# Kernel tuning notes

Hardware: AMD Instinct MI355X
Metric: run time of the kernel (lower is better)

## Reference

```python
import jax, jax.numpy as jnp
import numpy as np

B, N, D, H, L = 16, 1024, 256, 128, 2  # batch, nodes, feat dim, gcn_hidden, n_layers (D == 2*H)


def setup_inputs() -> dict:
    key = jax.random.key(0)
    ks = jax.random.split(key, 16)
    inp = {
        "gcn_input": jax.random.normal(ks[0], (B, N, D), jnp.float32),
        # scale adjacencies by 1/N so aggregated features stay O(1)
        "latent_adj": jax.random.uniform(ks[1], (B, N, N), jnp.float32) / N,
        "dep_adj": jax.random.uniform(ks[2], (B, N, N), jnp.float32) / N,
        # stacked per-layer parameters (leading dim L); layers share shapes since D == 2*H
        "refine_gate": jax.random.normal(ks[3], (L, D, 1), jnp.float32) * 0.02,
        "gate_W_in": jax.random.normal(ks[4], (L, D, 1), jnp.float32) * 0.02,
        "gate_b_in": jnp.zeros((L, 1), jnp.float32),
        "gate_W_out": jax.random.normal(ks[5], (L, D, 1), jnp.float32) * 0.02,
        "gate_b_out": jnp.zeros((L, 1), jnp.float32),
        "fc_in_W": jax.random.normal(ks[6], (L, H, D), jnp.float32) * 0.02,
        "fc_in_b": jnp.zeros((L, H), jnp.float32),
        "fc_out_W": jax.random.normal(ks[7], (L, H, D), jnp.float32) * 0.02,
        "fc_out_b": jnp.zeros((L, H), jnp.float32),
        "ln_g": jnp.ones((L, 2 * H), jnp.float32),
        "ln_b": jnp.zeros((L, 2 * H), jnp.float32),
    }
    return inp


def _gcn_layer(x, latent, dep, rg, Wgi, bgi, Wgo, bgo, Wi, bi, Wo, bo, g, b):
    # refine gate blends dependency and latent adjacency per source node
    gate = jax.nn.sigmoid(x @ rg)  # [B,N,1]
    A_in = gate * dep + (1.0 - gate) * latent  # [B,N,N]
    A_out = gate * jnp.swapaxes(dep, -1, -2) + (1.0 - gate) * jnp.swapaxes(latent, -1, -2)
    Ax_in = A_in @ x   # [B,N,D]
    Ax_out = A_out @ x
    # gcn gates (scalar bias added after the gated product, as in torch)
    Ax_in = Ax_in * jax.nn.sigmoid(Ax_in @ Wgi) + bgi
    Ax_out = Ax_out * jax.nn.sigmoid(Ax_out @ Wgo) + bgo
    # rec_fc(Ax) + rec_fc(x): weight applied to sum, bias counted twice (faithful)
    h_in = (Ax_in + x) @ Wi.T + 2.0 * bi   # [B,N,H]
    h_out = (Ax_out + x) @ Wo.T + 2.0 * bo
    h = jnp.concatenate([h_in, h_out], axis=-1)  # [B,N,2H]
    mu = jnp.mean(h, axis=-1, keepdims=True)
    var = jnp.var(h, axis=-1, keepdims=True)
    h = (h - mu) * jax.lax.rsqrt(var + 1e-5) * g + b
    return jax.nn.gelu(h, approximate=False)


def reference(gcn_input, latent_adj, dep_adj, refine_gate, gate_W_in, gate_b_in,
              gate_W_out, gate_b_out, fc_in_W, fc_in_b, fc_out_W, fc_out_b, ln_g, ln_b):
    x = gcn_input
    for l in range(refine_gate.shape[0]):  # small fixed layer count
        x = _gcn_layer(x, latent_adj, dep_adj, refine_gate[l],
                       gate_W_in[l], gate_b_in[l], gate_W_out[l], gate_b_out[l],
                       fc_in_W[l], fc_in_b[l], fc_out_W[l], fc_out_b[l],
                       ln_g[l], ln_b[l])
    return x
```

## Files before the change

### kernel.cpp

```cpp
#include <hip/hip_runtime.h>
#include <hip/hip_bf16.h>
#include <cstdint>

#define B_ 16
#define N_ 1024
#define D_ 256
#define H_ 128

typedef unsigned short u16;
typedef __attribute__((ext_vector_type(8))) short bf16x8;
typedef __attribute__((ext_vector_type(4))) short bf16x4;
typedef __attribute__((ext_vector_type(4))) float f32x4;

template<int V> struct IC { static constexpr int value = V; };

__device__ __forceinline__ u16 f2bf(float f) {
    union { float f; uint32_t u; } v; v.f = f;
    return (u16)((v.u + 0x7FFFu + ((v.u >> 16) & 1u)) >> 16);
}
__device__ __forceinline__ float bf2f(u16 h) {
    union { uint32_t u; float f; } v; v.u = ((uint32_t)h) << 16;
    return v.f;
}

typedef __attribute__((address_space(3))) void lds_void;
typedef const __attribute__((address_space(1))) void g_void;

__device__ __forceinline__ void gl_lds16(const void* g, void* l) {
    __builtin_amdgcn_global_load_lds((g_void*)g, (lds_void*)l, 16, 0, 0);
}

__device__ __forceinline__ void vm_wait6() { asm volatile("s_waitcnt vmcnt(6)" ::: "memory"); }
__device__ __forceinline__ void vm_wait3() { asm volatile("s_waitcnt vmcnt(3)" ::: "memory"); }
__device__ __forceinline__ void vm_wait2() { asm volatile("s_waitcnt vmcnt(2)" ::: "memory"); }
__device__ __forceinline__ void vm_wait0() { asm volatile("s_waitcnt vmcnt(0)" ::: "memory"); }
__device__ __forceinline__ void lgkm0()   { asm volatile("s_waitcnt lgkmcnt(0)" ::: "memory"); }
__device__ __forceinline__ void schedb()  { __builtin_amdgcn_sched_barrier(0); }

__global__ __launch_bounds__(256) void k_conv_adj(
    const float* __restrict__ dep, const float* __restrict__ lat,
    u16* __restrict__ depTb, u16* __restrict__ latTb)
{
    __shared__ u16 tile[64][64];
    const int bz = blockIdx.z;
    const int b = bz >> 1;
    const float* src = (bz & 1) ? lat : dep;
    u16* dstT = (bz & 1) ? latTb : depTb;
    const int r0 = blockIdx.y * 64, c0 = blockIdx.x * 64;
    const int t = threadIdx.x;
    const int r = t >> 2, cg = (t & 3) * 16;

    const float* srow = src + ((size_t)b * N_ + r0 + r) * N_ + c0 + cg;
    bf16x8 lo, hi;
    {
        const float4 v0 = *(const float4*)(srow);
        const float4 v1 = *(const float4*)(srow + 4);
        const float4 v2 = *(const float4*)(srow + 8);
        const float4 v3 = *(const float4*)(srow + 12);
        lo[0] = (short)f2bf(v0.x); lo[1] = (short)f2bf(v0.y); lo[2] = (short)f2bf(v0.z); lo[3] = (short)f2bf(v0.w);
        lo[4] = (short)f2bf(v1.x); lo[5] = (short)f2bf(v1.y); lo[6] = (short)f2bf(v1.z); lo[7] = (short)f2bf(v1.w);
        hi[0] = (short)f2bf(v2.x); hi[1] = (short)f2bf(v2.y); hi[2] = (short)f2bf(v2.z); hi[3] = (short)f2bf(v2.w);
        hi[4] = (short)f2bf(v3.x); hi[5] = (short)f2bf(v3.y); hi[6] = (short)f2bf(v3.z); hi[7] = (short)f2bf(v3.w);
    }

    const int g0 = (t & 3) * 2;
    const int s = r & 7;
    *(bf16x8*)(&tile[r][((g0    ) ^ s) * 8]) = lo;
    *(bf16x8*)(&tile[r][((g0 + 1) ^ s) * 8]) = hi;
    __syncthreads();

    const int sc = t >> 2, rg2 = (t & 3) * 16;
    bf16x8 o0, o1;
    #pragma unroll
    for (int i = 0; i < 8; ++i) {
        const int R = rg2 + i;
        o0[i] = (short)tile[R][(((sc >> 3) ^ (R & 7)) * 8) + (sc & 7)];
    }
    #pragma unroll
    for (int i = 0; i < 8; ++i) {
        const int R = rg2 + 8 + i;
        o1[i] = (short)tile[R][(((sc >> 3) ^ (R & 7)) * 8) + (sc & 7)];
    }
    u16* dT = dstT + ((size_t)b * N_ + c0 + sc) * N_ + r0 + rg2;
    *(bf16x8*)dT = o0;
    *(bf16x8*)(dT + 8) = o1;
}

__global__ __launch_bounds__(256) void k_gate_xt(
    const float* __restrict__ x, const float* __restrict__ rg,
    float* __restrict__ gate, u16* __restrict__ xT,
    const float* __restrict__ wi, const float* __restrict__ wo,
    u16* __restrict__ wib, u16* __restrict__ wob)
{
    if (blockIdx.y >= B_) {
        const int i = ((blockIdx.y - B_) * 32 + blockIdx.x) * 256 + threadIdx.x;
        wib[i] = f2bf(wi[i]);
        wob[i] = f2bf(wo[i]);
        return;
    }

    __shared__ u16 lx[D_][36];
    __shared__ float srg[D_];
    const int b = blockIdx.y, n0 = blockIdx.x * 32;
    const int t = threadIdx.x;
    srg[t] = rg[t];
    __syncthreads();

    const int r = t >> 3, cg = t & 7;
    const float* xrow = x + ((size_t)b * N_ + n0 + r) * D_;
    float dot = 0.f;
    #pragma unroll
    for (int u = 0; u < 8; ++u) {
        const int c = cg * 32 + u * 4;
        const float4 v = *(const float4*)(xrow + c);
        lx[c][r] = f2bf(v.x); lx[c + 1][r] = f2bf(v.y);
        lx[c + 2][r] = f2bf(v.z); lx[c + 3][r] = f2bf(v.w);
        dot += v.x * srg[c] + v.y * srg[c + 1] + v.z * srg[c + 2] + v.w * srg[c + 3];
    }
    dot += __shfl_down(dot, 4, 8);
    dot += __shfl_down(dot, 2, 8);
    dot += __shfl_down(dot, 1, 8);
    if (cg == 0) gate[(size_t)b * N_ + n0 + r] = 1.f / (1.f + expf(-dot));
    __syncthreads();

    #pragma unroll
    for (int i = 0; i < 8; ++i) {
        const int unit = i * 256 + t;
        const int d = unit >> 3, nch = (unit & 7) * 4;
        ushort4 wv;
        wv.x = lx[d][nch];     wv.y = lx[d][nch + 1];
        wv.z = lx[d][nch + 2]; wv.w = lx[d][nch + 3];
        *(ushort4*)(xT + ((size_t)b * D_ + d) * N_ + n0 + nch) = wv;
    }
}

__global__ __launch_bounds__(512, 2) void k_gemm_ax(
    const float* __restrict__ depf, const float* __restrict__ latf,
    const u16* __restrict__ depTb, const u16* __restrict__ latTb,
    const u16* __restrict__ xT,
    const float* __restrict__ gate,
    const float* __restrict__ Wgi, const float* __restrict__ Wgo,
    const float* __restrict__ bgi, const float* __restrict__ bgo,
    const float* __restrict__ xcur,
    u16* __restrict__ axin, u16* __restrict__ axout)
{
    __shared__ __align__(16) char smem[51712];
    u16* const sb = (u16*)smem;
    float* hbuf = (float*)smem;
    float* psum = (float*)(smem + 49152);
    float* sh_s = (float*)(smem + 51200);

    const int bid = blockIdx.x;
    const int logical = (bid & 7) * 32 + (bid >> 3);
    const int b = logical >> 4;
    const int rem = logical & 15;
    const int z = rem >> 3;
    const int m0 = (rem & 7) * 128;

    const float* Wg = z ? Wgo : Wgi;
    const float bg0 = z ? bgo[0] : bgi[0];
    u16* outp = z ? axout : axin;

    const int t = threadIdx.x;
    const int lane = t & 63;
    const int w = t >> 6;
    const int wr = w >> 2, wc = w & 3;

    const int arow = t >> 2;
    const int akq = t & 3;
    const float gv = gate[(size_t)b * N_ + m0 + arow];
    const int awoff = arow * 32 + ((akq ^ ((arow >> 1) & 3)) << 3);
    const float* gD = depf + ((size_t)b * N_ + m0 + arow) * N_ + akq * 8;
    const float* gL = latf + ((size_t)b * N_ + m0 + arow) * N_ + akq * 8;
    const u16* gT1 = depTb + ((size_t)b * N_ + m0 + arow) * N_ + akq * 8;
    const u16* gT2 = latTb + ((size_t)b * N_ + m0 + arow) * N_ + akq * 8;

    const int rl = lane >> 2;
    const int kk = (((lane & 3) ^ ((lane >> 3) & 3)) << 3);
    const u16* gB0 = xT + ((size_t)b * D_ + (w * 2) * 16 + rl) * N_ + kk;
    const u16* gB1 = xT + ((size_t)b * D_ + (w * 2 + 1) * 16 + rl) * N_ + kk;
    const int boff0 = 4096 + (w * 2) * 512;
    const int boff1 = 4096 + (w * 2 + 1) * 512;

    const int mrow = lane & 15;
    const int hi = lane >> 4;
    const int kg = (((lane >> 4) ^ ((mrow >> 1) & 3)) << 3);

    f32x4 acc[4][4];
    const f32x4 fz = {0.f, 0.f, 0.f, 0.f};
    #pragma unroll
    for (int i = 0; i < 4; ++i)
        #pragma unroll
        for (int j = 0; j < 4; ++j) acc[i][j] = fz;

    struct RegsF { float4 d0, d1, l0, l1; };
    struct RegsH { bf16x4 a0, a1, b0, b1; };

    auto run = [&](auto zc) {
        constexpr int Z = decltype(zc)::value;

        auto LOAD = [&](auto& r, int ks) {
            if constexpr (Z == 0) {
                r.d0 = *(const float4*)(gD + ks * 32);
                r.d1 = *(const float4*)(gD + ks * 32 + 4);
                r.l0 = *(const float4*)(gL + ks * 32);
                r.l1 = *(const float4*)(gL + ks * 32 + 4);
            } else {
                r.a0 = *(const bf16x4*)(gT1 + ks * 32);
                r.a1 = *(const bf16x4*)(gT1 + ks * 32 + 4);
                r.b0 = *(const bf16x4*)(gT2 + ks * 32);
                r.b1 = *(const bf16x4*)(gT2 + ks * 32 + 4);
            }
        };
        auto BLEND = [&](const auto& r, u16* dst) {
            bf16x8 bl;
            if constexpr (Z == 0) {
                bl[0] = (short)f2bf(r.l0.x + gv * (r.d0.x - r.l0.x));
                bl[1] = (short)f2bf(r.l0.y + gv * (r.d0.y - r.l0.y));
                bl[2] = (short)f2bf(r.l0.z + gv * (r.d0.z - r.l0.z));
                bl[3] = (short)f2bf(r.l0.w + gv * (r.d0.w - r.l0.w));
                bl[4] = (short)f2bf(r.l1.x + gv * (r.d1.x - r.l1.x));
                bl[5] = (short)f2bf(r.l1.y + gv * (r.d1.y - r.l1.y));
                bl[6] = (short)f2bf(r.l1.z + gv * (r.d1.z - r.l1.z));
                bl[7] = (short)f2bf(r.l1.w + gv * (r.d1.w - r.l1.w));
            } else {
                #pragma unroll
                for (int u = 0; u < 4; ++u) {
                    const float f1 = bf2f((u16)r.a0[u]);
                    const float f2 = bf2f((u16)r.b0[u]);
                    bl[u] = (short)f2bf(f2 + gv * (f1 - f2));
                }
                #pragma unroll
                for (int u = 0; u < 4; ++u) {
                    const float f1 = bf2f((u16)r.a1[u]);
                    const float f2 = bf2f((u16)r.b1[u]);
                    bl[4 + u] = (short)f2bf(f2 + gv * (f1 - f2));
                }
            }
            *(bf16x8*)dst = bl;
        };

        auto body = [&](int ks, auto& c, auto& n) {
            if (ks <= 28) LOAD(n, ks + 3);
            const u16* sA = sb + (ks & 1) * 12288;
            const u16* sBc = sA + 4096;
            bf16x8 a[4], fbv[4];
            #pragma unroll
            for (int mt = 0; mt < 4; ++mt)
                a[mt] = *(const bf16x8*)(sA + (wr * 64 + mt * 16 + mrow) * 32 + kg);
            #pragma unroll
            for (int nt = 0; nt < 4; ++nt)
                fbv[nt] = *(const bf16x8*)(sBc + (wc * 64 + nt * 16 + mrow) * 32 + kg);
            #pragma unroll
            for (int mt = 0; mt < 4; ++mt)
                #pragma unroll
                for (int nt = 0; nt < 4; ++nt)
                    acc[mt][nt] = __builtin_amdgcn_mfma_f32_16x16x32_bf16(a[mt], fbv[nt], acc[mt][nt], 0, 0, 0);
            schedb();
            __builtin_amdgcn_s_barrier();
            schedb();
            if (ks <= 29) {
                u16* cb = sb + (ks & 1) * 12288;
                BLEND(c, cb + awoff);
                gl_lds16(gB0 + (ks + 2) * 32, cb + boff0);
                gl_lds16(gB1 + (ks + 2) * 32, cb + boff1);
            }
            if (ks <= 28) vm_wait6();
            else if (ks == 29) vm_wait2();
            else if (ks == 30) vm_wait0();
            lgkm0();
            schedb();
            __builtin_amdgcn_s_barrier();
            schedb();
        };

        typename std::conditional<Z == 0, RegsF, RegsH>::type x, y;
        LOAD(x, 0); BLEND(x, sb + awoff);
        LOAD(y, 1); BLEND(y, sb + 12288 + awoff);
        LOAD(x, 2);
        gl_lds16(gB0, sb + boff0);          gl_lds16(gB1, sb + boff1);
        gl_lds16(gB0 + 32, sb + 12288 + boff0); gl_lds16(gB1 + 32, sb + 12288 + boff1);
        vm_wait2();
        lgkm0();
        schedb(); __builtin_amdgcn_s_barrier(); schedb();

        for (int kp = 0; kp < 16; ++kp) {
            body(2 * kp, x, y);
            body(2 * kp + 1, y, x);
        }
    };
    if (z == 0) run(IC<0>()); else run(IC<1>());
    __syncthreads();

    float wgv[4];
    #pragma unroll
    for (int nt = 0; nt < 4; ++nt) wgv[nt] = Wg[wc * 64 + nt * 16 + mrow];
    #pragma unroll
    for (int mt = 0; mt < 4; ++mt) {
        #pragma unroll
        for (int rr = 0; rr < 4; ++rr) {
            float p = acc[mt][0][rr] * wgv[0] + acc[mt][1][rr] * wgv[1]
                    + acc[mt][2][rr] * wgv[2] + acc[mt][3][rr] * wgv[3];
            p += __shfl_xor(p, 1, 16);
            p += __shfl_xor(p, 2, 16);
            p += __shfl_xor(p, 4, 16);
            p += __shfl_xor(p, 8, 16);
            if (mrow == 0) psum[(wr * 64 + mt * 16 + hi * 4 + rr) * 4 + wc] = p;
        }
    }
    __syncthreads();
    if (t < 128) {
        const float d = psum[t * 4] + psum[t * 4 + 1] + psum[t * 4 + 2] + psum[t * 4 + 3];
        sh_s[t] = 1.f / (1.f + expf(-d));
    }
    __syncthreads();

    #pragma unroll
    for (int p = 0; p < 4; ++p) {
        if (wr == (p >> 1)) {
            #pragma unroll
            for (int mtl = 0; mtl < 2; ++mtl) {
                const int mt = (p & 1) * 2 + mtl;
                #pragma unroll
                for (int nt = 0; nt < 4; ++nt) {
                    const int col = wc * 64 + nt * 16 + mrow;
                    #pragma unroll
                    for (int rr = 0; rr < 4; ++rr) {
                        const int hrow = mtl * 16 + hi * 4 + rr;
                        hbuf[hrow * 260 + col] = acc[mt][nt][rr];
                    }
                }
            }
        }
        __syncthreads();
        {
            const int sr = t >> 4;
            const int sc0 = (t & 15) * 16;
            const int grow = p * 32 + sr;
            const float s = sh_s[grow];
            const size_t gb = ((size_t)b * N_ + m0 + grow) * D_ + sc0;
            const float* xr = xcur + gb;
            u16* orow = outp + gb;
            bf16x8 o0, o1;
            #pragma unroll
            for (int u = 0; u < 8; ++u)
                o0[u] = (short)f2bf(hbuf[sr * 260 + sc0 + u] * s + bg0 + xr[u]);
            #pragma unroll
            for (int u = 0; u < 8; ++u)
                o1[u] = (short)f2bf(hbuf[sr * 260 + sc0 + 8 + u] * s + bg0 + xr[8 + u]);
            *(bf16x8*)orow = o0;
            *(bf16x8*)(orow + 8) = o1;
        }
        __syncthreads();
    }
}

__global__ __launch_bounds__(512, 2) void k_fc_ln(
    const u16* __restrict__ axin, const u16* __restrict__ axout,
    const u16* __restrict__ Wib, const u16* __restrict__ Wob,
    const float* __restrict__ bi, const float* __restrict__ bo,
    const float* __restrict__ lg, const float* __restrict__ lb,
    float* __restrict__ outp)
{
    __shared__ __align__(16) char smem[51712];
    u16* const sb = (u16*)smem;
    float* hbuf = (float*)smem;
    float* psum = (float*)(smem + 49152);
    float* sh_mu = (float*)(smem + 51200);
    float* sh_rs = (float*)(smem + 51456);

    const int bid = blockIdx.x;
    const int logical = (bid & 7) * 32 + (bid >> 3);
    const int b = logical >> 4;
    const int m0 = (logical & 15) * 64;

    const int t = threadIdx.x, lane = t & 63, w = t >> 6;
    const int wr = w >> 2, wc = w & 3;
    const int half = wc >> 1;

    const int rl = lane >> 2;
    const int kk = (((lane & 3) ^ ((lane >> 3) & 3)) << 3);

    const u16* gsrc[3];
    int loff[3];
    #pragma unroll
    for (int ci = 0; ci < 3; ++ci) {
        const int c = w * 3 + ci;
        if (c < 4) {
            gsrc[ci] = axin + ((size_t)b * N_ + m0 + c * 16 + rl) * D_ + kk;
            loff[ci] = c * 512;
        } else if (c < 8) {
            gsrc[ci] = axout + ((size_t)b * N_ + m0 + (c - 4) * 16 + rl) * D_ + kk;
            loff[ci] = 2048 + (c - 4) * 512;
        } else {
            const int cw = c - 8;
            const u16* base = (cw < 8) ? (Wib + (size_t)(cw * 16 + rl) * D_)
                                       : (Wob + (size_t)((cw - 8) * 16 + rl) * D_);
            gsrc[ci] = base + kk;
            loff[ci] = 4096 + cw * 512;
        }
    }

    f32x4 acc[2][4];
    const f32x4 fz = {0.f, 0.f, 0.f, 0.f};
    #pragma unroll
    for (int i = 0; i < 2; ++i)
        #pragma unroll
        for (int j = 0; j < 4; ++j) acc[i][j] = fz;

    #pragma unroll
    for (int ci = 0; ci < 3; ++ci) gl_lds16(gsrc[ci], sb + loff[ci]);
    #pragma unroll
    for (int ci = 0; ci < 3; ++ci) gl_lds16(gsrc[ci] + 32, sb + 12288 + loff[ci]);
    vm_wait3();
    lgkm0();
    schedb(); __builtin_amdgcn_s_barrier(); schedb();

    const int mrow = lane & 15;
    const int hi = lane >> 4;
    const int kg = (((lane >> 4) ^ ((mrow >> 1) & 3)) << 3);

    for (int ks = 0; ks < 8; ++ks) {
        const u16* cur = sb + (ks & 1) * 12288;
        const u16* sA = cur + (half ? 2048 : 0);
        const u16* sW = cur + 4096;
        bf16x8 a[2], fbv[4];
        #pragma unroll
        for (int mt = 0; mt < 2; ++mt)
            a[mt] = *(const bf16x8*)(sA + (wr * 32 + mt * 16 + mrow) * 32 + kg);
        #pragma unroll
        for (int nt = 0; nt < 4; ++nt)
            fbv[nt] = *(const bf16x8*)(sW + (wc * 64 + nt * 16 + mrow) * 32 + kg);
        #pragma unroll
        for (int mt = 0; mt < 2; ++mt)
            #pragma unroll
            for (int nt = 0; nt < 4; ++nt)
                acc[mt][nt] = __builtin_amdgcn_mfma_f32_16x16x32_bf16(a[mt], fbv[nt], acc[mt][nt], 0, 0, 0);
        schedb();
        __builtin_amdgcn_s_barrier();
        schedb();
        if (ks <= 5) {
            u16* nb = sb + (ks & 1) * 12288;
            #pragma unroll
            for (int ci = 0; ci < 3; ++ci) gl_lds16(gsrc[ci] + (ks + 2) * 32, nb + loff[ci]);
        }
        if (ks <= 5) vm_wait3();
        else if (ks == 6) vm_wait0();
        lgkm0();
        schedb();
        __builtin_amdgcn_s_barrier();
        schedb();
    }
    __syncthreads();

    float bc[4];
    #pragma unroll
    for (int nt = 0; nt < 4; ++nt) {
        const int colh = wc * 64 + nt * 16 + mrow;
        bc[nt] = 2.f * (colh < 128 ? bi[colh] : bo[colh - 128]);
    }
    #pragma unroll
    for (int mt = 0; mt < 2; ++mt)
        #pragma unroll
        for (int rr = 0; rr < 4; ++rr) {
            const int lrow = wr * 32 + mt * 16 + hi * 4 + rr;
            float s = 0.f, ss = 0.f;
            #pragma unroll
            for (int nt = 0; nt < 4; ++nt) {
                const float v = acc[mt][nt][rr] + bc[nt];
                s += v; ss += v * v;
            }
            s += __shfl_xor(s, 1, 16);  ss += __shfl_xor(ss, 1, 16);
            s += __shfl_xor(s, 2, 16);  ss += __shfl_xor(ss, 2, 16);
            s += __shfl_xor(s, 4, 16);  ss += __shfl_xor(ss, 4, 16);
            s += __shfl_xor(s, 8, 16);  ss += __shfl_xor(ss, 8, 16);
            if (mrow == 0) {
                psum[lrow * 8 + wc * 2] = s;
                psum[lrow * 8 + wc * 2 + 1] = ss;
            }
        }
    __syncthreads();
    if (t < 64) {
        const float s = psum[t * 8] + psum[t * 8 + 2] + psum[t * 8 + 4] + psum[t * 8 + 6];
        const float ss = psum[t * 8 + 1] + psum[t * 8 + 3] + psum[t * 8 + 5] + psum[t * 8 + 7];
        const float mu = s * (1.f / 256.f);
        const float var = ss * (1.f / 256.f) - mu * mu;
        sh_mu[t] = mu;
        sh_rs[t] = rsqrtf(var + 1e-5f);
    }
    __syncthreads();

    #pragma unroll
    for (int p = 0; p < 2; ++p) {
        if (wr == p) {
            #pragma unroll
            for (int mt = 0; mt < 2; ++mt)
                #pragma unroll
                for (int nt = 0; nt < 4; ++nt) {
                    const int col = wc * 64 + nt * 16 + mrow;
                    #pragma unroll
                    for (int rr = 0; rr < 4; ++rr) {
                        const int hrow = mt * 16 + hi * 4 + rr;
                        hbuf[hrow * 260 + col] = acc[mt][nt][rr] + bc[nt];
                    }
                }
        }
        __syncthreads();
        {
            const int sr = t >> 4;
            const int sc0 = (t & 15) * 16;
            const int grow = p * 32 + sr;
            const float mu = sh_mu[grow], rs = sh_rs[grow];
            float* orow = outp + ((size_t)b * N_ + m0 + grow) * D_ + sc0;
            #pragma unroll
            for (int q = 0; q < 4; ++q) {
                const float4 gg = *(const float4*)(lg + sc0 + q * 4);
                const float4 bb = *(const float4*)(lb + sc0 + q * 4);
                float4 o;
                const float v0 = (hbuf[sr * 260 + sc0 + q * 4    ] - mu) * rs * gg.x + bb.x;
                const float v1 = (hbuf[sr * 260 + sc0 + q * 4 + 1] - mu) * rs * gg.y + bb.y;
                const float v2 = (hbuf[sr * 260 + sc0 + q * 4 + 2] - mu) * rs * gg.z + bb.z;
                const float v3 = (hbuf[sr * 260 + sc0 + q * 4 + 3] - mu) * rs * gg.w + bb.w;
                o.x = 0.5f * v0 * (1.f + erff(v0 * 0.70710678118654752f));
                o.y = 0.5f * v1 * (1.f + erff(v1 * 0.70710678118654752f));
                o.z = 0.5f * v2 * (1.f + erff(v2 * 0.70710678118654752f));
                o.w = 0.5f * v3 * (1.f + erff(v3 * 0.70710678118654752f));
                *(float4*)(orow + q * 4) = o;
            }
        }
        __syncthreads();
    }
}

extern "C" void kernel_launch(void* const* d_in, const int* in_sizes, int n_in,
                              void* d_out, int out_size, void* d_ws, size_t ws_size,
                              hipStream_t stream)
{
    (void)in_sizes; (void)n_in; (void)out_size; (void)ws_size;

    const float* x0  = (const float*)d_in[0];
    const float* lat = (const float*)d_in[1];
    const float* dep = (const float*)d_in[2];
    const float* rg  = (const float*)d_in[3];
    const float* Wgi = (const float*)d_in[4];
    const float* bgi = (const float*)d_in[5];
    const float* Wgo = (const float*)d_in[6];
    const float* bgo = (const float*)d_in[7];
    const float* fiW = (const float*)d_in[8];
    const float* fib = (const float*)d_in[9];
    const float* foW = (const float*)d_in[10];
    const float* fob = (const float*)d_in[11];
    const float* lng = (const float*)d_in[12];
    const float* lnb = (const float*)d_in[13];

    char* ws = (char*)d_ws;
    size_t off = 0;
    auto alloc = [&](size_t bytes) {
        char* p = ws + off;
        off += (bytes + 255) & ~(size_t)255;
        return p;
    };
    u16* depTb = (u16*)alloc(2ull * B_ * N_ * N_);
    u16* latTb = (u16*)alloc(2ull * B_ * N_ * N_);
    u16* xT    = (u16*)alloc(2ull * B_ * D_ * N_);
    u16* axin  = (u16*)alloc(2ull * B_ * N_ * D_);
    u16* axout = (u16*)alloc(2ull * B_ * N_ * D_);
    float* gate = (float*)alloc(4ull * B_ * N_);
    float* xbuf = (float*)alloc(4ull * B_ * N_ * D_);
    u16* Wib = (u16*)alloc(2ull * H_ * D_);
    u16* Wob = (u16*)alloc(2ull * H_ * D_);

    k_conv_adj<<<dim3(16, 16, 32), 256, 0, stream>>>(dep, lat, depTb, latTb);

    const float* xcur = x0;
    for (int l = 0; l < 2; ++l) {
        k_gate_xt<<<dim3(32, B_ + 4), 256, 0, stream>>>(
            xcur, rg + l * D_, gate, xT,
            fiW + (size_t)l * H_ * D_, foW + (size_t)l * H_ * D_, Wib, Wob);
        k_gemm_ax<<<dim3(256), 512, 0, stream>>>(
            dep, lat, depTb, latTb, xT, gate,
            Wgi + l * D_, Wgo + l * D_, bgi + l, bgo + l,
            xcur, axin, axout);
        const bool last = (l == 1);
        k_fc_ln<<<dim3(256), 512, 0, stream>>>(
            axin, axout, Wib, Wob,
            fib + l * H_, fob + l * H_,
            lng + l * 2 * H_, lnb + l * 2 * H_,
            last ? (float*)d_out : xbuf);
        xcur = xbuf;
    }
}
```

Before: 336.6 us.

## Precompute bf16 non-transposed adjacency so both GEMM paths stream bf16

The conversion kernel now also writes a bf16 copy of dep and lat in their original layout, and the Ax GEMM reads that instead of fp32 for the A_in path. Both paths now share one code path with 16-byte bf16 loads, halving the per-layer A traffic for the z=0 half, at the cost of an extra bf16 write of both adjacencies once up front. The LDS transpose swizzle was also changed to XOR in higher row bits to reduce bank conflicts, and the wait count was adjusted for fewer outstanding loads.

```diff
diff --git a/kernel.cpp b/kernel.cpp
--- a/kernel.cpp
+++ b/kernel.cpp
@@ -9,10 +9,7 @@
 
 typedef unsigned short u16;
 typedef __attribute__((ext_vector_type(8))) short bf16x8;
-typedef __attribute__((ext_vector_type(4))) short bf16x4;
 typedef __attribute__((ext_vector_type(4))) float f32x4;
-
-template<int V> struct IC { static constexpr int value = V; };
 
 __device__ __forceinline__ u16 f2bf(float f) {
     union { float f; uint32_t u; } v; v.f = f;
@@ -30,7 +27,7 @@
     __builtin_amdgcn_global_load_lds((g_void*)g, (lds_void*)l, 16, 0, 0);
 }
 
-__device__ __forceinline__ void vm_wait6() { asm volatile("s_waitcnt vmcnt(6)" ::: "memory"); }
+__device__ __forceinline__ void vm_wait4() { asm volatile("s_waitcnt vmcnt(4)" ::: "memory"); }
 __device__ __forceinline__ void vm_wait3() { asm volatile("s_waitcnt vmcnt(3)" ::: "memory"); }
 __device__ __forceinline__ void vm_wait2() { asm volatile("s_waitcnt vmcnt(2)" ::: "memory"); }
 __device__ __forceinline__ void vm_wait0() { asm volatile("s_waitcnt vmcnt(0)" ::: "memory"); }
@@ -39,12 +36,14 @@
 
 __global__ __launch_bounds__(256) void k_conv_adj(
     const float* __restrict__ dep, const float* __restrict__ lat,
+    u16* __restrict__ depb, u16* __restrict__ latb,
     u16* __restrict__ depTb, u16* __restrict__ latTb)
 {
     __shared__ u16 tile[64][64];
     const int bz = blockIdx.z;
     const int b = bz >> 1;
     const float* src = (bz & 1) ? lat : dep;
+    u16* dstN = (bz & 1) ? latb : depb;
     u16* dstT = (bz & 1) ? latTb : depTb;
     const int r0 = blockIdx.y * 64, c0 = blockIdx.x * 64;
     const int t = threadIdx.x;
@@ -62,9 +61,12 @@
         hi[0] = (short)f2bf(v2.x); hi[1] = (short)f2bf(v2.y); hi[2] = (short)f2bf(v2.z); hi[3] = (short)f2bf(v2.w);
         hi[4] = (short)f2bf(v3.x); hi[5] = (short)f2bf(v3.y); hi[6] = (short)f2bf(v3.z); hi[7] = (short)f2bf(v3.w);
     }
+    u16* nrow = dstN + ((size_t)b * N_ + r0 + r) * N_ + c0 + cg;
+    *(bf16x8*)nrow = lo;
+    *(bf16x8*)(nrow + 8) = hi;
 
     const int g0 = (t & 3) * 2;
-    const int s = r & 7;
+    const int s = (r & 7) ^ ((r >> 3) & 7);
     *(bf16x8*)(&tile[r][((g0    ) ^ s) * 8]) = lo;
     *(bf16x8*)(&tile[r][((g0 + 1) ^ s) * 8]) = hi;
     __syncthreads();
@@ -74,12 +76,14 @@
     #pragma unroll
     for (int i = 0; i < 8; ++i) {
         const int R = rg2 + i;
-        o0[i] = (short)tile[R][(((sc >> 3) ^ (R & 7)) * 8) + (sc & 7)];
+        const int sR = (R & 7) ^ ((R >> 3) & 7);
+        o0[i] = (short)tile[R][(((sc >> 3) ^ sR) * 8) + (sc & 7)];
     }
     #pragma unroll
     for (int i = 0; i < 8; ++i) {
         const int R = rg2 + 8 + i;
-        o1[i] = (short)tile[R][(((sc >> 3) ^ (R & 7)) * 8) + (sc & 7)];
+        const int sR = (R & 7) ^ ((R >> 3) & 7);
+        o1[i] = (short)tile[R][(((sc >> 3) ^ sR) * 8) + (sc & 7)];
     }
     u16* dT = dstT + ((size_t)b * N_ + c0 + sc) * N_ + r0 + rg2;
     *(bf16x8*)dT = o0;
@@ -135,7 +139,7 @@
 }
 
 __global__ __launch_bounds__(512, 2) void k_gemm_ax(
-    const float* __restrict__ depf, const float* __restrict__ latf,
+    const u16* __restrict__ depb, const u16* __restrict__ latb,
     const u16* __restrict__ depTb, const u16* __restrict__ latTb,
     const u16* __restrict__ xT,
     const float* __restrict__ gate,
@@ -157,6 +161,8 @@
     const int z = rem >> 3;
     const int m0 = (rem & 7) * 128;
 
+    const u16* A1 = z ? depTb : depb;
+    const u16* A2 = z ? latTb : latb;
     const float* Wg = z ? Wgo : Wgi;
     const float bg0 = z ? bgo[0] : bgi[0];
     u16* outp = z ? axout : axin;
@@ -169,11 +175,9 @@
     const int arow = t >> 2;
     const int akq = t & 3;
     const float gv = gate[(size_t)b * N_ + m0 + arow];
+    const u16* gA1 = A1 + ((size_t)b * N_ + m0 + arow) * N_ + akq * 8;
+    const u16* gA2 = A2 + ((size_t)b * N_ + m0 + arow) * N_ + akq * 8;
     const int awoff = arow * 32 + ((akq ^ ((arow >> 1) & 3)) << 3);
-    const float* gD = depf + ((size_t)b * N_ + m0 + arow) * N_ + akq * 8;
-    const float* gL = latf + ((size_t)b * N_ + m0 + arow) * N_ + akq * 8;
-    const u16* gT1 = depTb + ((size_t)b * N_ + m0 + arow) * N_ + akq * 8;
-    const u16* gT2 = latTb + ((size_t)b * N_ + m0 + arow) * N_ + akq * 8;
 
     const int rl = lane >> 2;
     const int kk = (((lane & 3) ^ ((lane >> 3) & 3)) << 3);
@@ -193,103 +197,71 @@
         #pragma unroll
         for (int j = 0; j < 4; ++j) acc[i][j] = fz;
 
-    struct RegsF { float4 d0, d1, l0, l1; };
-    struct RegsH { bf16x4 a0, a1, b0, b1; };
-
-    auto run = [&](auto zc) {
-        constexpr int Z = decltype(zc)::value;
-
-        auto LOAD = [&](auto& r, int ks) {
-            if constexpr (Z == 0) {
-                r.d0 = *(const float4*)(gD + ks * 32);
-                r.d1 = *(const float4*)(gD + ks * 32 + 4);
-                r.l0 = *(const float4*)(gL + ks * 32);
-                r.l1 = *(const float4*)(gL + ks * 32 + 4);
-            } else {
-                r.a0 = *(const bf16x4*)(gT1 + ks * 32);
-                r.a1 = *(const bf16x4*)(gT1 + ks * 32 + 4);
-                r.b0 = *(const bf16x4*)(gT2 + ks * 32);
-                r.b1 = *(const bf16x4*)(gT2 + ks * 32 + 4);
-            }
-        };
-        auto BLEND = [&](const auto& r, u16* dst) {
-            bf16x8 bl;
-            if constexpr (Z == 0) {
-                bl[0] = (short)f2bf(r.l0.x + gv * (r.d0.x - r.l0.x));
-                bl[1] = (short)f2bf(r.l0.y + gv * (r.d0.y - r.l0.y));
-                bl[2] = (short)f2bf(r.l0.z + gv * (r.d0.z - r.l0.z));
-                bl[3] = (short)f2bf(r.l0.w + gv * (r.d0.w - r.l0.w));
-                bl[4] = (short)f2bf(r.l1.x + gv * (r.d1.x - r.l1.x));
-                bl[5] = (short)f2bf(r.l1.y + gv * (r.d1.y - r.l1.y));
-                bl[6] = (short)f2bf(r.l1.z + gv * (r.d1.z - r.l1.z));
-                bl[7] = (short)f2bf(r.l1.w + gv * (r.d1.w - r.l1.w));
-            } else {
-                #pragma unroll
-                for (int u = 0; u < 4; ++u) {
-                    const float f1 = bf2f((u16)r.a0[u]);
-                    const float f2 = bf2f((u16)r.b0[u]);
-                    bl[u] = (short)f2bf(f2 + gv * (f1 - f2));
-                }
-                #pragma unroll
-                for (int u = 0; u < 4; ++u) {
-                    const float f1 = bf2f((u16)r.a1[u]);
-                    const float f2 = bf2f((u16)r.b1[u]);
-                    bl[4 + u] = (short)f2bf(f2 + gv * (f1 - f2));
-                }
-            }
-            *(bf16x8*)dst = bl;
-        };
-
-        auto body = [&](int ks, auto& c, auto& n) {
-            if (ks <= 28) LOAD(n, ks + 3);
-            const u16* sA = sb + (ks & 1) * 12288;
-            const u16* sBc = sA + 4096;
-            bf16x8 a[4], fbv[4];
-            #pragma unroll
-            for (int mt = 0; mt < 4; ++mt)
-                a[mt] = *(const bf16x8*)(sA + (wr * 64 + mt * 16 + mrow) * 32 + kg);
+    bf16x8 rA1x, rA2x, rA1y, rA2y;
+
+    auto blend_store = [&](const bf16x8& a1v, const bf16x8& a2v, u16* dst) {
+        bf16x8 bl;
+        #pragma unroll
+        for (int u = 0; u < 8; ++u) {
+            const float f1 = bf2f((u16)a1v[u]);
+            const float f2 = bf2f((u16)a2v[u]);
+            bl[u] = (short)f2bf(f2 + gv * (f1 - f2));
+        }
+        *(bf16x8*)dst = bl;
+    };
+
+    rA1x = *(const bf16x8*)(gA1);       rA2x = *(const bf16x8*)(gA2);
+    blend_store(rA1x, rA2x, sb + awoff);
+    rA1x = *(const bf16x8*)(gA1 + 32);  rA2x = *(const bf16x8*)(gA2 + 32);
+    gl_lds16(gB0, sb + boff0);          gl_lds16(gB1, sb + boff1);
+    blend_store(rA1x, rA2x, sb + 12288 + awoff);
+    rA1x = *(const bf16x8*)(gA1 + 64);  rA2x = *(const bf16x8*)(gA2 + 64);
+    gl_lds16(gB0 + 32, sb + 12288 + boff0); gl_lds16(gB1 + 32, sb + 12288 + boff1);
+    vm_wait2();
+    lgkm0();
+    schedb(); __builtin_amdgcn_s_barrier(); schedb();
+
+    auto body = [&](int ks, bf16x8& c1, bf16x8& c2, bf16x8& n1, bf16x8& n2) {
+        if (ks <= 28) {
+            n1 = *(const bf16x8*)(gA1 + (ks + 3) * 32);
+            n2 = *(const bf16x8*)(gA2 + (ks + 3) * 32);
+        }
+        const u16* sA = sb + (ks & 1) * 12288;
+        const u16* sBc = sA + 4096;
+        bf16x8 a[4], fbv[4];
+        #pragma unroll
+        for (int mt = 0; mt < 4; ++mt)
+            a[mt] = *(const bf16x8*)(sA + (wr * 64 + mt * 16 + mrow) * 32 + kg);
+        #pragma unroll
+        for (int nt = 0; nt < 4; ++nt)
+            fbv[nt] = *(const bf16x8*)(sBc + (wc * 64 + nt * 16 + mrow) * 32 + kg);
+        #pragma unroll
+        for (int mt = 0; mt < 4; ++mt)
             #pragma unroll
             for (int nt = 0; nt < 4; ++nt)
-                fbv[nt] = *(const bf16x8*)(sBc + (wc * 64 + nt * 16 + mrow) * 32 + kg);
-            #pragma unroll
-            for (int mt = 0; mt < 4; ++mt)
-                #pragma unroll
-                for (int nt = 0; nt < 4; ++nt)
-                    acc[mt][nt] = __builtin_amdgcn_mfma_f32_16x16x32_bf16(a[mt], fbv[nt], acc[mt][nt], 0, 0, 0);
-            schedb();
-            __builtin_amdgcn_s_barrier();
-            schedb();
-            if (ks <= 29) {
-                u16* cb = sb + (ks & 1) * 12288;
-                BLEND(c, cb + awoff);
-                gl_lds16(gB0 + (ks + 2) * 32, cb + boff0);
-                gl_lds16(gB1 + (ks + 2) * 32, cb + boff1);
-            }
-            if (ks <= 28) vm_wait6();
-            else if (ks == 29) vm_wait2();
-            else if (ks == 30) vm_wait0();
-            lgkm0();
-            schedb();
-            __builtin_amdgcn_s_barrier();
-            schedb();
-        };
-
-        typename std::conditional<Z == 0, RegsF, RegsH>::type x, y;
-        LOAD(x, 0); BLEND(x, sb + awoff);
-        LOAD(y, 1); BLEND(y, sb + 12288 + awoff);
-        LOAD(x, 2);
-        gl_lds16(gB0, sb + boff0);          gl_lds16(gB1, sb + boff1);
-        gl_lds16(gB0 + 32, sb + 12288 + boff0); gl_lds16(gB1 + 32, sb + 12288 + boff1);
-        vm_wait2();
+                acc[mt][nt] = __builtin_amdgcn_mfma_f32_16x16x32_bf16(a[mt], fbv[nt], acc[mt][nt], 0, 0, 0);
+        schedb();
+        __builtin_amdgcn_s_barrier();
+        schedb();
+        if (ks <= 29) {
+            u16* cb = sb + (ks & 1) * 12288;
+            blend_store(c1, c2, cb + awoff);
+            gl_lds16(gB0 + (ks + 2) * 32, cb + boff0);
+            gl_lds16(gB1 + (ks + 2) * 32, cb + boff1);
+        }
+        if (ks <= 28) vm_wait4();
+        else if (ks == 29) vm_wait2();
+        else if (ks == 30) vm_wait0();
         lgkm0();
-        schedb(); __builtin_amdgcn_s_barrier(); schedb();
-
-        for (int kp = 0; kp < 16; ++kp) {
-            body(2 * kp, x, y);
-            body(2 * kp + 1, y, x);
-        }
+        schedb();
+        __builtin_amdgcn_s_barrier();
+        schedb();
     };
-    if (z == 0) run(IC<0>()); else run(IC<1>());
+
+    for (int kp = 0; kp < 16; ++kp) {
+        body(2 * kp,     rA1x, rA2x, rA1y, rA2y);
+        body(2 * kp + 1, rA1y, rA2y, rA1x, rA2x);
+    }
     __syncthreads();
 
     float wgv[4];
@@ -560,6 +532,8 @@
         off += (bytes + 255) & ~(size_t)255;
         return p;
     };
+    u16* depb  = (u16*)alloc(2ull * B_ * N_ * N_);
+    u16* latb  = (u16*)alloc(2ull * B_ * N_ * N_);
     u16* depTb = (u16*)alloc(2ull * B_ * N_ * N_);
     u16* latTb = (u16*)alloc(2ull * B_ * N_ * N_);
     u16* xT    = (u16*)alloc(2ull * B_ * D_ * N_);
@@ -570,7 +544,7 @@
     u16* Wib = (u16*)alloc(2ull * H_ * D_);
     u16* Wob = (u16*)alloc(2ull * H_ * D_);
 
-    k_conv_adj<<<dim3(16, 16, 32), 256, 0, stream>>>(dep, lat, depTb, latTb);
+    k_conv_adj<<<dim3(16, 16, 32), 256, 0, stream>>>(dep, lat, depb, latb, depTb, latTb);
 
     const float* xcur = x0;
     for (int l = 0; l < 2; ++l) {
@@ -578,7 +552,7 @@
             xcur, rg + l * D_, gate, xT,
             fiW + (size_t)l * H_ * D_, foW + (size_t)l * H_ * D_, Wib, Wob);
         k_gemm_ax<<<dim3(256), 512, 0, stream>>>(
-            dep, lat, depTb, latTb, xT, gate,
+            depb, latb, depTb, latTb, xT, gate,
             Wgi + l * D_, Wgo + l * D_, bgi + l, bgo + l,
             xcur, axin, axout);
         const bool last = (l == 1);
```

Result: faster. 323.2 us (-4.0%).
